# Optimization experiments

Measured on AMD Instinct MI355X. Metric: run time of the kernel, lower is better.

## Reference

```python
import jax, jax.numpy as jnp
import numpy as np

D_STATE = 8
DT_RANK = 8  # ceil(128/16)


def _grouped_1x1(x, w):
    # x: (B,H,W,Cin), w: (g, Cout//g, Cin//g)
    B, H, W, _ = x.shape
    g, o, i = w.shape
    xg = x.reshape(B, H, W, g, i)
    return jnp.einsum('bhwgi,goi->bhwgo', xg, w).reshape(B, H, W, g * o)


def setup_inputs() -> dict:
    key = jax.random.key(0)
    ks = jax.random.split(key, 16)
    B, H, W, C = 8, 64, 64, 128
    g = 4
    D = 128  # expand_dim = d_inner
    N = D_STATE
    R = DT_RANK
    inp = {}
    inp['x'] = jax.random.normal(ks[0], (B, H, W, C), dtype=jnp.float32)
    inp['w1'] = jax.random.normal(ks[1], (g, D // g, C // g), dtype=jnp.float32) * 0.1
    inp['dw'] = jax.random.normal(ks[2], (3, 3, 1, D), dtype=jnp.float32) * 0.1  # HWIO depthwise
    inp['in_proj_w'] = jax.random.normal(ks[3], (2 * D, D), dtype=jnp.float32) * 0.05
    inp['conv1d_w'] = jax.random.normal(ks[4], (D, 3), dtype=jnp.float32) * 0.1
    inp['conv1d_b'] = jax.random.normal(ks[5], (D,), dtype=jnp.float32) * 0.05
    inp['x_proj_w'] = jax.random.normal(ks[6], (R + 2 * N, D), dtype=jnp.float32) * 0.05
    inp['dt_proj_w'] = jax.random.normal(ks[7], (D, R), dtype=jnp.float32) * 0.05
    inp['dt_proj_b'] = jax.random.normal(ks[8], (D,), dtype=jnp.float32) * 0.05
    inp['A_log'] = jnp.log(jnp.tile(jnp.arange(1, N + 1, dtype=jnp.float32)[None, :], (D, 1)))
    inp['D_param'] = jnp.ones((D,), dtype=jnp.float32)
    inp['out_proj_w'] = jax.random.normal(ks[9], (D, D), dtype=jnp.float32) * 0.05
    inp['gamma'] = jnp.ones((D,), dtype=jnp.float32)
    inp['beta'] = jnp.zeros((D,), dtype=jnp.float32)
    inp['w2'] = jax.random.normal(ks[10], (g, D // g, C // g), dtype=jnp.float32) * 0.1
    inp['wout'] = jax.random.normal(ks[11], (g, C // g, D // g), dtype=jnp.float32) * 0.1
    return inp


def _mamba(x_seq, in_proj_w, conv1d_w, conv1d_b, x_proj_w, dt_proj_w, dt_proj_b, A_log, D_param, out_proj_w):
    # x_seq: (B, L, D)
    B, L, D = x_seq.shape
    N, R = D_STATE, DT_RANK
    xz = jnp.einsum('bld,ed->ble', x_seq, in_proj_w)  # (B,L,2D)
    u, z = xz[..., :D], xz[..., D:]
    # causal depthwise conv1d, kernel=3, left pad 2 (torch: padding=2, slice [:L])
    up = jnp.pad(u, ((0, 0), (2, 0), (0, 0)))
    u = (up[:, 0:L] * conv1d_w[:, 0] + up[:, 1:L + 1] * conv1d_w[:, 1]
         + up[:, 2:L + 2] * conv1d_w[:, 2] + conv1d_b)
    u = jax.nn.silu(u)
    x_dbl = jnp.einsum('bld,ed->ble', u, x_proj_w)  # (B,L,R+2N)
    dt = x_dbl[..., :R]
    Bm = x_dbl[..., R:R + N]
    Cm = x_dbl[..., R + N:]
    delta = jax.nn.softplus(jnp.einsum('blr,dr->bld', dt, dt_proj_w) + dt_proj_b)  # (B,L,D)
    A = -jnp.exp(A_log)  # (D,N)

    def step(h, inp):
        d_t, u_t, b_t, c_t = inp  # (B,D),(B,D),(B,N),(B,N)
        dA = jnp.exp(d_t[..., None] * A)            # (B,D,N)
        h = dA * h + (d_t * u_t)[..., None] * b_t[:, None, :]
        y_t = jnp.einsum('bdn,bn->bd', h, c_t)
        return h, y_t

    h0 = jnp.zeros((B, D, N), dtype=x_seq.dtype)
    xs = (jnp.swapaxes(delta, 0, 1), jnp.swapaxes(u, 0, 1),
          jnp.swapaxes(Bm, 0, 1), jnp.swapaxes(Cm, 0, 1))
    _, ys = jax.lax.scan(step, h0, xs)              # ys: (L,B,D)
    y = jnp.swapaxes(ys, 0, 1) + u * D_param
    y = y * jax.nn.silu(z)
    return jnp.einsum('bld,ed->ble', y, out_proj_w)


def reference(x, w1, dw, in_proj_w, conv1d_w, conv1d_b, x_proj_w, dt_proj_w, dt_proj_b,
              A_log, D_param, out_proj_w, gamma, beta, w2, wout):
    B, H, W, C = x.shape
    D = dw.shape[-1]
    x1 = _grouped_1x1(x, w1)  # (B,H,W,D)
    x1 = jax.lax.conv_general_dilated(
        x1, dw, window_strides=(1, 1), padding='SAME',
        feature_group_count=D, dimension_numbers=('NHWC', 'HWIO', 'NHWC'))
    x1 = jax.nn.silu(x1)
    x1_seq = x1.reshape(B, H * W, D)
    x1_seq = _mamba(x1_seq, in_proj_w, conv1d_w, conv1d_b, x_proj_w,
                    dt_proj_w, dt_proj_b, A_log, D_param, out_proj_w)
    x1 = x1_seq.reshape(B, H, W, D)
    mu = jnp.mean(x1, axis=-1, keepdims=True)
    var = jnp.mean(jnp.square(x1 - mu), axis=-1, keepdims=True)
    x1 = (x1 - mu) * jax.lax.rsqrt(var + 1e-5) * gamma + beta
    x2 = jax.nn.silu(_grouped_1x1(x, w2))
    x_fuse = x1 * x2
    return _grouped_1x1(x_fuse, wout)  # (B,H,W,C)
```

## Files before the change

kernel.cpp:

```cpp
#include <hip/hip_runtime.h>
#include <math.h>

#define B_    8
#define C_    128
#define D_    128
#define L_    4096
#define NPOS_ 32768
#define NC_   256
#define S_    16
#define MFL_  1048576

typedef __attribute__((ext_vector_type(8))) short short8;
typedef __attribute__((ext_vector_type(4))) float f32x4;

__device__ __forceinline__ float siluf(float x) { return x / (1.f + __expf(-x)); }
__device__ __forceinline__ float softplusf(float x) {
    if (x > 20.f) return x;
    return __logf(1.f + __expf(x));
}
__device__ __forceinline__ unsigned short f2bf(float f) {
    unsigned int u = __float_as_uint(f);
    u = (u + 0x7FFFu + ((u >> 16) & 1u)) >> 16;
    return (unsigned short)u;
}
__device__ __forceinline__ float bf2f(unsigned short h) {
    return __uint_as_float(((unsigned int)h) << 16);
}
__device__ __forceinline__ void scan_as(float dl, const float* Ar, bool fast, float* a) {
    if (fast) {
        float e1 = __expf(-dl);
        a[0] = e1;
        a[1] = e1 * e1;
        a[2] = a[1] * e1;
        a[3] = a[1] * a[1];
        a[4] = a[3] * e1;
        a[5] = a[3] * a[1];
        a[6] = a[5] * e1;
        a[7] = a[3] * a[3];
    } else {
        #pragma unroll
        for (int n = 0; n < 8; ++n) a[n] = __expf(dl * Ar[n]);
    }
}

__global__ __launch_bounds__(256) void k1_g1x1(const float* __restrict__ x,
                                               const float* __restrict__ w1,
                                               const float* __restrict__ w2,
                                               const float* __restrict__ inW,
                                               const float* __restrict__ OW,
                                               const float* __restrict__ xpw,
                                               unsigned short* __restrict__ inWb,
                                               unsigned short* __restrict__ OWb,
                                               unsigned short* __restrict__ xpwb,
                                               unsigned short* __restrict__ t1b,
                                               unsigned short* __restrict__ x2sb) {
    __shared__ float xs[16 * 128];
    int t = threadIdx.x;
    {
        int i = blockIdx.x * 51 + t;
        if (t < 51 && i < 52224) {
            if (i < 32768)      inWb[i] = f2bf(inW[i]);
            else if (i < 49152) OWb[i - 32768] = f2bf(OW[i - 32768]);
            else                xpwb[i - 49152] = f2bf(xpw[i - 49152]);
        }
    }
    int op = t & 63, ph = t >> 6;
    int g = op >> 4, o2 = (op & 15) * 2;
    const float* w1p = &w1[g * 1024 + o2 * 32];
    const float* w2p = &w2[g * 1024 + o2 * 32];
    float w1r[64], w2r[64];
    #pragma unroll
    for (int i = 0; i < 64; ++i) { w1r[i] = w1p[i]; w2r[i] = w2p[i]; }
    int pos0 = blockIdx.x * 32;
    for (int it = 0; it < 2; ++it) {
        int p0 = pos0 + it * 16;
        #pragma unroll
        for (int q = 0; q < 2; ++q) {
            int fi = t * 2 + q;
            *(float4*)&xs[fi * 4] = *(const float4*)&x[p0 * 128 + fi * 4];
        }
        __syncthreads();
        #pragma unroll
        for (int q = 0; q < 4; ++q) {
            int pl = ph * 4 + q;
            float a1 = 0.f, b1 = 0.f, a2 = 0.f, b2 = 0.f;
            const float* xr = &xs[pl * 128 + g * 32];
            #pragma unroll
            for (int i4 = 0; i4 < 8; ++i4) {
                float4 xv = *(const float4*)&xr[i4 * 4];
                a1 += xv.x * w1r[i4*4]    + xv.y * w1r[i4*4+1]    + xv.z * w1r[i4*4+2]    + xv.w * w1r[i4*4+3];
                b1 += xv.x * w1r[32+i4*4] + xv.y * w1r[32+i4*4+1] + xv.z * w1r[32+i4*4+2] + xv.w * w1r[32+i4*4+3];
                a2 += xv.x * w2r[i4*4]    + xv.y * w2r[i4*4+1]    + xv.z * w2r[i4*4+2]    + xv.w * w2r[i4*4+3];
                b2 += xv.x * w2r[32+i4*4] + xv.y * w2r[32+i4*4+1] + xv.z * w2r[32+i4*4+2] + xv.w * w2r[32+i4*4+3];
            }
            int pos = p0 + pl;
            int db = pos * 128 + g * 32 + o2;
            unsigned int u1 = (unsigned int)f2bf(a1) | ((unsigned int)f2bf(b1) << 16);
            unsigned int u2 = (unsigned int)f2bf(siluf(a2)) | ((unsigned int)f2bf(siluf(b2)) << 16);
            *(unsigned int*)&t1b[db]  = u1;
            *(unsigned int*)&x2sb[db] = u2;
        }
        __syncthreads();
    }
}

__global__ __launch_bounds__(128) void k2_dwconv(const unsigned short* __restrict__ t1b,
                                                 const float* __restrict__ dw,
                                                 unsigned short* __restrict__ x1cb) {
    int d = threadIdx.x;
    float dwr[9];
    #pragma unroll
    for (int k = 0; k < 9; ++k) dwr[k] = dw[k * 128 + d];
    int bid = blockIdx.x;
    int wt = bid & 15, ht = (bid >> 4) & 7, b = bid >> 7;
    int h0 = ht * 8, w0 = wt * 4;
    float rows[10][6];
    #pragma unroll
    for (int r = 0; r < 10; ++r) {
        int hh = h0 - 1 + r;
        bool hv = (hh >= 0) && (hh < 64);
        #pragma unroll
        for (int c = 0; c < 6; ++c) {
            int w = w0 - 1 + c;
            bool wvv = (w >= 0) && (w < 64);
            rows[r][c] = (hv && wvv) ? bf2f(t1b[((b * 64 + hh) * 64 + w) * 128 + d]) : 0.f;
        }
    }
    #pragma unroll
    for (int hi = 0; hi < 8; ++hi) {
        #pragma unroll
        for (int wi = 0; wi < 4; ++wi) {
            float acc = rows[hi][wi]     * dwr[0] + rows[hi][wi+1]   * dwr[1] + rows[hi][wi+2]   * dwr[2]
                      + rows[hi+1][wi]   * dwr[3] + rows[hi+1][wi+1] * dwr[4] + rows[hi+1][wi+2] * dwr[5]
                      + rows[hi+2][wi]   * dwr[6] + rows[hi+2][wi+1] * dwr[7] + rows[hi+2][wi+2] * dwr[8];
            x1cb[((b * 64 + h0 + hi) * 64 + w0 + wi) * 128 + d] = f2bf(siluf(acc));
        }
    }
}

__global__ __launch_bounds__(256) void k3_mfma(const unsigned short* __restrict__ Abf,
                                               const unsigned short* __restrict__ Bbf,
                                               unsigned short* __restrict__ urawb,
                                               unsigned short* __restrict__ zb) {
    __shared__ unsigned short Al[64 * 72];
    __shared__ unsigned short Bl[128 * 72];
    int t = threadIdx.x;
    int pos0 = (blockIdx.x >> 1) * 64;
    int half = blockIdx.x & 1;
    const unsigned short* Bh = Bbf + (size_t)half * 128 * 128;
    unsigned short* dst = half ? zb : urawb;
    int lane = t & 63, wv = t >> 6;
    int lanem = lane & 15, laneq = lane >> 4;
    f32x4 acc[8];
    #pragma unroll
    for (int i = 0; i < 8; ++i) acc[i] = (f32x4){0.f, 0.f, 0.f, 0.f};
    for (int kc = 0; kc < 2; ++kc) {
        #pragma unroll
        for (int q = 0; q < 2; ++q) {
            int c = t + q * 256;
            int row = c >> 3, col = c & 7;
            *(int4*)&Al[row * 72 + col * 8] = *(const int4*)&Abf[(pos0 + row) * 128 + kc * 64 + col * 8];
        }
        #pragma unroll
        for (int q = 0; q < 4; ++q) {
            int c = t + q * 256;
            int row = c >> 3, col = c & 7;
            *(int4*)&Bl[row * 72 + col * 8] = *(const int4*)&Bh[row * 128 + kc * 64 + col * 8];
        }
        __syncthreads();
        #pragma unroll
        for (int ks = 0; ks < 2; ++ks) {
            short8 af = *(const short8*)&Al[(wv * 16 + lanem) * 72 + ks * 32 + laneq * 8];
            #pragma unroll
            for (int ni = 0; ni < 8; ++ni) {
                short8 bfr = *(const short8*)&Bl[(ni * 16 + lanem) * 72 + ks * 32 + laneq * 8];
                acc[ni] = __builtin_amdgcn_mfma_f32_16x16x32_bf16(af, bfr, acc[ni], 0, 0, 0);
            }
        }
        __syncthreads();
    }
    #pragma unroll
    for (int ni = 0; ni < 8; ++ni)
        #pragma unroll
        for (int r = 0; r < 4; ++r) {
            int m = pos0 + wv * 16 + laneq * 4 + r;
            int n = ni * 16 + lanem;
            dst[m * 128 + n] = f2bf(acc[ni][r]);
        }
}

__global__ __launch_bounds__(256) void k45_convproj(const unsigned short* __restrict__ urawb,
                                                    const float* __restrict__ cw,
                                                    const float* __restrict__ cb,
                                                    const unsigned short* __restrict__ xpwb,
                                                    const float* __restrict__ dtw,
                                                    const float* __restrict__ dtb,
                                                    const float* __restrict__ A_log,
                                                    unsigned short* __restrict__ usb,
                                                    unsigned short* __restrict__ deltab,
                                                    float* __restrict__ Bm,
                                                    float* __restrict__ Cm,
                                                    float* __restrict__ cA,
                                                    float* __restrict__ cB) {
    __shared__ unsigned short uA[32 * 136];
    __shared__ unsigned short xB[32 * 136];
    __shared__ float xdb[32 * 36];
    int t = threadIdx.x;
    int d = t & 127, ph = t >> 7;
    for (int i = t; i < 32 * 128; i += 256) {
        int n = i >> 7, k = i & 127;
        xB[n * 136 + k] = (n < 24) ? xpwb[n * 128 + k] : (unsigned short)0;
    }
    float cw0 = cw[d * 3 + 0], cw1 = cw[d * 3 + 1], cw2 = cw[d * 3 + 2], cbr = cb[d];
    float dtwr[8];
    #pragma unroll
    for (int r = 0; r < 8; ++r) dtwr[r] = dtw[d * 8 + r];
    float dtbr = dtb[d];
    float Ar[8]; bool fast = true;
    #pragma unroll
    for (int n = 0; n < 8; ++n) {
        Ar[n] = -__expf(A_log[d * 8 + n]);
        fast = fast && (fabsf(Ar[n] + (float)(n + 1)) < 2e-3f);
    }

    int gpos0 = blockIdx.x * 32;
    int ll0 = (gpos0 & 4095) + ph * 16;
    int base = (gpos0 + ph * 16) * 128 + d;
    float ur0 = (ll0 >= 2) ? bf2f(urawb[base - 256]) : 0.f;
    float ur1 = (ll0 >= 1) ? bf2f(urawb[base - 128]) : 0.f;
    #pragma unroll
    for (int q = 0; q < 16; ++q) {
        float urq = bf2f(urawb[base + q * 128]);
        float v = siluf(ur0 * cw0 + ur1 * cw1 + urq * cw2 + cbr);
        unsigned short vb = f2bf(v);
        usb[base + q * 128] = vb;
        uA[(ph * 16 + q) * 136 + d] = vb;
        ur0 = ur1; ur1 = urq;
    }
    __syncthreads();
    int lane = t & 63, wv = t >> 6;
    int lanem = lane & 15, laneq = lane >> 4;
    int m0 = (wv & 1) * 16, n0 = (wv >> 1) * 16;
    f32x4 accx = (f32x4){0.f, 0.f, 0.f, 0.f};
    #pragma unroll
    for (int ks = 0; ks < 4; ++ks) {
        short8 af  = *(const short8*)&uA[(m0 + lanem) * 136 + ks * 32 + laneq * 8];
        short8 bfr = *(const short8*)&xB[(n0 + lanem) * 136 + ks * 32 + laneq * 8];
        accx = __builtin_amdgcn_mfma_f32_16x16x32_bf16(af, bfr, accx, 0, 0, 0);
    }
    #pragma unroll
    for (int r = 0; r < 4; ++r)
        xdb[(m0 + laneq * 4 + r) * 36 + n0 + lanem] = accx[r];
    __syncthreads();
    float h[8], ap[8];
    #pragma unroll
    for (int n = 0; n < 8; ++n) { h[n] = 0.f; ap[n] = 1.f; }
    #pragma unroll
    for (int q = 0; q < 16; ++q) {
        int pl = ph * 16 + q;
        const float* xrow = &xdb[pl * 36];
        float4 d0 = *(const float4*)&xrow[0];
        float4 d1 = *(const float4*)&xrow[4];
        float dt = dtbr + d0.x * dtwr[0] + d0.y * dtwr[1] + d0.z * dtwr[2] + d0.w * dtwr[3]
                        + d1.x * dtwr[4] + d1.y * dtwr[5] + d1.z * dtwr[6] + d1.w * dtwr[7];
        unsigned short dlb = f2bf(softplusf(dt));
        deltab[base + q * 128] = dlb;
        float dl = bf2f(dlb);
        float du = dl * bf2f(uA[pl * 136 + d]);
        float bmv[8];
        *(float4*)&bmv[0] = *(const float4*)&xrow[8];
        *(float4*)&bmv[4] = *(const float4*)&xrow[12];
        float a[8];
        scan_as(dl, Ar, fast, a);
        #pragma unroll
        for (int n = 0; n < 8; ++n) {
            ap[n] *= a[n];
            h[n] = a[n] * h[n] + du * bmv[n];
        }
    }
    int bH = gpos0 >> 12;
    int c  = ((gpos0 & 4095) >> 4) + ph;
    int obase = ((bH * NC_ + c) * 128 + d) * 8;
    *(float4*)&cA[obase]     = make_float4(ap[0], ap[1], ap[2], ap[3]);
    *(float4*)&cA[obase + 4] = make_float4(ap[4], ap[5], ap[6], ap[7]);
    *(float4*)&cB[obase]     = make_float4(h[0], h[1], h[2], h[3]);
    *(float4*)&cB[obase + 4] = make_float4(h[4], h[5], h[6], h[7]);
    if (t < 128) {
        int p = t >> 2, q = t & 3;
        float4 v = *(const float4*)&xdb[p * 36 + 8 + q * 4];
        int gp = gpos0 + p;
        if (q < 2) *(float4*)&Bm[gp * 8 + q * 4] = v;
        else       *(float4*)&Cm[gp * 8 + (q - 2) * 4] = v;
    }
}

__global__ __launch_bounds__(256) void k6a_scan(float* __restrict__ cA,
                                                float* __restrict__ cB,
                                                float* __restrict__ AgA,
                                                float* __restrict__ AgB) {
    int id = blockIdx.x * 256 + threadIdx.x;
    int dn = id & 1023;
    int grp = (id >> 10) & 15;
    int b = id >> 14;
    float Apre = 1.f, h = 0.f;
    int base = (b * NC_ + grp * 16) * 1024 + dn;
    #pragma unroll 4
    for (int j = 0; j < 16; ++j) {
        int idx = base + j * 1024;
        float a  = cA[idx];
        float bv = cB[idx];
        cA[idx] = Apre;
        cB[idx] = h;
        Apre *= a;
        h = a * h + bv;
    }
    int aidx = (b * 16 + grp) * 1024 + dn;
    AgA[aidx] = Apre;
    AgB[aidx] = h;
}

__global__ __launch_bounds__(256) void k6b_scan(const float* __restrict__ AgA,
                                                const float* __restrict__ AgB,
                                                float* __restrict__ gcar) {
    int id = blockIdx.x * 256 + threadIdx.x;
    int dn = id & 1023;
    int b = id >> 10;
    float h = 0.f;
    #pragma unroll
    for (int grp = 0; grp < 16; ++grp) {
        int idx = (b * 16 + grp) * 1024 + dn;
        float Ag = AgA[idx];
        float Bg = AgB[idx];
        gcar[idx] = h;
        h = Ag * h + Bg;
    }
}

__global__ __launch_bounds__(512) void k7f_fused(const unsigned short* __restrict__ deltab,
                                                 const unsigned short* __restrict__ usb,
                                                 const float* __restrict__ Bm,
                                                 const float* __restrict__ Cm,
                                                 const unsigned short* __restrict__ zb,
                                                 const float* __restrict__ A_log,
                                                 const float* __restrict__ Dp,
                                                 const float* __restrict__ Apre,
                                                 const float* __restrict__ Bpre,
                                                 const float* __restrict__ gcar,
                                                 const unsigned short* __restrict__ OWb,
                                                 const float* __restrict__ gamma,
                                                 const float* __restrict__ beta,
                                                 const unsigned short* __restrict__ x2sb,
                                                 const float* __restrict__ wout,
                                                 float* __restrict__ out) {
    __shared__ __align__(16) char smem[37888];
    unsigned short* yA = (unsigned short*)smem;
    unsigned short* Bl = (unsigned short*)(smem + 18432);
    float* xz = (float*)smem;
    __shared__ float woutL[4 * 1160];
    __shared__ float gbL[256];
    int t = threadIdx.x;
    for (int idx = t; idx < 4096; idx += 512) {
        int g = idx >> 10, r = idx & 1023, o = r >> 5, i = r & 31;
        woutL[g * 1160 + o * 36 + i] = wout[idx];
    }
    if (t < 128) gbL[t] = gamma[t];
    else if (t < 256) gbL[t] = beta[t - 128];

    int d = t & 127, ph = t >> 7;
    int b = blockIdx.x >> 6, cblk = blockIdx.x & 63;
    float Ar[8]; bool fast = true;
    #pragma unroll
    for (int n = 0; n < 8; ++n) {
        Ar[n] = -__expf(A_log[d * 8 + n]);
        fast = fast && (fabsf(Ar[n] + (float)(n + 1)) < 2e-3f);
    }
    float Dpr = Dp[d];
    int ybase = (d >> 6) * (64 * 72) + (d & 63);
    {
        int cl = ph;
        int c = cblk * 4 + cl;
        int cbase = ((b * NC_ + c) * 128 + d) * 8;
        float4 ap0 = *(const float4*)&Apre[cbase];
        float4 ap1 = *(const float4*)&Apre[cbase + 4];
        float4 bp0 = *(const float4*)&Bpre[cbase];
        float4 bp1 = *(const float4*)&Bpre[cbase + 4];
        int gbase = (b * 16 + (c >> 4)) * 1024 + d * 8;
        float4 g0 = *(const float4*)&gcar[gbase];
        float4 g1 = *(const float4*)&gcar[gbase + 4];
        float h[8] = { fmaf(g0.x, ap0.x, bp0.x), fmaf(g0.y, ap0.y, bp0.y),
                       fmaf(g0.z, ap0.z, bp0.z), fmaf(g0.w, ap0.w, bp0.w),
                       fmaf(g1.x, ap1.x, bp1.x), fmaf(g1.y, ap1.y, bp1.y),
                       fmaf(g1.z, ap1.z, bp1.z), fmaf(g1.w, ap1.w, bp1.w) };
        int base  = (b * L_ + c * S_) * 128 + d;
        int bbase = (b * L_ + c * S_) * 8;
        #pragma unroll
        for (int s = 0; s < S_; ++s) {
            float dl = bf2f(deltab[base + s * 128]);
            float uv = bf2f(usb[base + s * 128]);
            float zv = bf2f(zb[base + s * 128]);
            float du = dl * uv;
            float4 bm0 = *(const float4*)&Bm[bbase + s * 8];
            float4 bm1 = *(const float4*)&Bm[bbase + s * 8 + 4];
            float4 cm0 = *(const float4*)&Cm[bbase + s * 8];
            float4 cm1 = *(const float4*)&Cm[bbase + s * 8 + 4];
            float a[8];
            scan_as(dl, Ar, fast, a);
            h[0] = a[0] * h[0] + du * bm0.x;
            h[1] = a[1] * h[1] + du * bm0.y;
            h[2] = a[2] * h[2] + du * bm0.z;
            h[3] = a[3] * h[3] + du * bm0.w;
            h[4] = a[4] * h[4] + du * bm1.x;
            h[5] = a[5] * h[5] + du * bm1.y;
            h[6] = a[6] * h[6] + du * bm1.z;
            h[7] = a[7] * h[7] + du * bm1.w;
            float yv = h[0] * cm0.x + h[1] * cm0.y + h[2] * cm0.z + h[3] * cm0.w
                     + h[4] * cm1.x + h[5] * cm1.y + h[6] * cm1.z + h[7] * cm1.w;
            yv = (yv + uv * Dpr) * siluf(zv);
            yA[ybase + (cl * 16 + s) * 72] = f2bf(yv);
        }
    }
    __syncthreads();

    int lane = t & 63, wv = t >> 6;
    int lanem = lane & 15, laneq = lane >> 4;
    int mi = wv & 3, nb = (wv >> 2) * 4;
    f32x4 acc[4];
    #pragma unroll
    for (int i = 0; i < 4; ++i) acc[i] = (f32x4){0.f, 0.f, 0.f, 0.f};
    for (int kc = 0; kc < 2; ++kc) {
        #pragma unroll
        for (int q = 0; q < 2; ++q) {
            int cidx = t + q * 512;
            int row = cidx >> 3, col = cidx & 7;
            *(int4*)&Bl[row * 72 + col * 8] = *(const int4*)&OWb[row * 128 + kc * 64 + col * 8];
        }
        __syncthreads();
        #pragma unroll
        for (int ks = 0; ks < 2; ++ks) {
            short8 af = *(const short8*)&yA[kc * (64 * 72) + (mi * 16 + lanem) * 72 + ks * 32 + laneq * 8];
            #pragma unroll
            for (int ni = 0; ni < 4; ++ni) {
                short8 bfr = *(const short8*)&Bl[((nb + ni) * 16 + lanem) * 72 + ks * 32 + laneq * 8];
                acc[ni] = __builtin_amdgcn_mfma_f32_16x16x32_bf16(af, bfr, acc[ni], 0, 0, 0);
            }
        }
        __syncthreads();
    }
    #pragma unroll
    for (int ni = 0; ni < 4; ++ni) {
        int ch = (nb + ni) * 16 + lanem;
        int col = ch + ((ch >> 5) << 2);
        #pragma unroll
        for (int r = 0; r < 4; ++r)
            xz[(mi * 16 + laneq * 4 + r) * 148 + col] = bf2f(f2bf(acc[ni][r]));
    }
    __syncthreads();

    if (t < 256) {
        int g = t & 3, pos = t >> 2;
        int gpos = b * L_ + cblk * 64 + pos;
        const float* xrow0 = &xz[pos * 148 + g * 36];
        float v[32];
        #pragma unroll
        for (int i4 = 0; i4 < 8; ++i4) {
            float4 xv = *(const float4*)&xrow0[i4 * 4];
            v[i4*4+0] = xv.x; v[i4*4+1] = xv.y;
            v[i4*4+2] = xv.z; v[i4*4+3] = xv.w;
        }
        float s = 0.f, s2 = 0.f;
        #pragma unroll
        for (int i = 0; i < 32; ++i) { s += v[i]; s2 += v[i] * v[i]; }
        s  += __shfl_xor(s, 1, 64);  s  += __shfl_xor(s, 2, 64);
        s2 += __shfl_xor(s2, 1, 64); s2 += __shfl_xor(s2, 2, 64);
        float m = s * (1.f / 128.f);
        float var = s2 * (1.f / 128.f) - m * m;
        float rstd = rsqrtf(var + 1e-5f);
        #pragma unroll
        for (int i4 = 0; i4 < 8; ++i4) {
            ushort4 xv = *(const ushort4*)&x2sb[gpos * 128 + g * 32 + i4 * 4];
            unsigned short xa[4] = {xv.x, xv.y, xv.z, xv.w};
            #pragma unroll
            for (int k = 0; k < 4; ++k) {
                int e = g * 32 + i4 * 4 + k;
                float vv = (v[i4 * 4 + k] - m) * rstd * gbL[e] + gbL[128 + e];
                v[i4 * 4 + k] = vv * bf2f(xa[k]);
            }
        }
        const float* wg = &woutL[g * 1160];
        int obase = gpos * 128 + g * 32;
        #pragma unroll
        for (int ob = 0; ob < 8; ++ob) {
            float o4[4];
            #pragma unroll
            for (int oo = 0; oo < 4; ++oo) {
                int o = ob * 4 + oo;
                float acc2 = 0.f;
                #pragma unroll
                for (int i4 = 0; i4 < 8; ++i4) {
                    float4 wv4 = *(const float4*)&wg[o * 36 + i4 * 4];
                    acc2 += v[i4*4] * wv4.x + v[i4*4+1] * wv4.y
                          + v[i4*4+2] * wv4.z + v[i4*4+3] * wv4.w;
                }
                o4[oo] = acc2;
            }
            *(float4*)&out[obase + ob * 4] = make_float4(o4[0], o4[1], o4[2], o4[3]);
        }
    }
}

extern "C" void kernel_launch(void* const* d_in, const int* in_sizes, int n_in,
                              void* d_out, int out_size, void* d_ws, size_t ws_size,
                              hipStream_t stream) {
    (void)in_sizes; (void)n_in; (void)out_size; (void)ws_size;
    const float* x         = (const float*)d_in[0];
    const float* w1        = (const float*)d_in[1];
    const float* dw        = (const float*)d_in[2];
    const float* in_proj_w = (const float*)d_in[3];
    const float* conv1d_w  = (const float*)d_in[4];
    const float* conv1d_b  = (const float*)d_in[5];
    const float* x_proj_w  = (const float*)d_in[6];
    const float* dt_proj_w = (const float*)d_in[7];
    const float* dt_proj_b = (const float*)d_in[8];
    const float* A_log     = (const float*)d_in[9];
    const float* D_param   = (const float*)d_in[10];
    const float* out_proj_w= (const float*)d_in[11];
    const float* gamma     = (const float*)d_in[12];
    const float* beta      = (const float*)d_in[13];
    const float* w2        = (const float*)d_in[14];
    const float* wout      = (const float*)d_in[15];
    float* out = (float*)d_out;

    float* ws = (float*)d_ws;
    unsigned short* x2sb   = (unsigned short*)(ws);
    unsigned short* t1b    = (unsigned short*)(ws + 2  * (size_t)MFL_);
    unsigned short* x1cb   = (unsigned short*)(ws + 4  * (size_t)MFL_);
    unsigned short* urawb  = (unsigned short*)(ws + 6  * (size_t)MFL_);
    unsigned short* zb     = (unsigned short*)(ws + 8  * (size_t)MFL_);
    unsigned short* usb    = (unsigned short*)(ws + 14 * (size_t)MFL_);
    unsigned short* deltab = (unsigned short*)(ws + 16 * (size_t)MFL_);
    float* Bm    = ws + 18 * (size_t)MFL_;
    float* Cm    = Bm + (size_t)NPOS_ * 8;
    float* cA    = Cm + (size_t)NPOS_ * 8;
    float* cB    = cA + 2 * (size_t)MFL_;
    float* scanw = cB + 2 * (size_t)MFL_;
    float* AgA   = scanw;
    float* AgB   = scanw + 131072;
    float* gcar  = scanw + 262144;
    unsigned short* inWb = (unsigned short*)(scanw + 2 * (size_t)MFL_);
    unsigned short* OWb  = inWb + 32768;
    unsigned short* xpwb = OWb + 16384;

    k1_g1x1<<<1024, 256, 0, stream>>>(x, w1, w2, in_proj_w, out_proj_w, x_proj_w,
                                      inWb, OWb, xpwb, t1b, x2sb);
    k2_dwconv<<<1024, 128, 0, stream>>>(t1b, dw, x1cb);
    k3_mfma<<<1024, 256, 0, stream>>>(x1cb, inWb, urawb, zb);
    k45_convproj<<<1024, 256, 0, stream>>>(urawb, conv1d_w, conv1d_b, xpwb,
                                           dt_proj_w, dt_proj_b, A_log,
                                           usb, deltab, Bm, Cm, cA, cB);
    k6a_scan<<<512, 256, 0, stream>>>(cA, cB, AgA, AgB);
    k6b_scan<<<32, 256, 0, stream>>>(AgA, AgB, gcar);
    k7f_fused<<<512, 512, 0, stream>>>(deltab, usb, Bm, Cm, zb, A_log, D_param,
                                       cA, cB, gcar, OWb, gamma, beta, x2sb, wout, out);
}
```

Measured before the change: 213.4 us.

## Fuse depthwise conv into in_proj MFMA kernel via shared-memory A tile

Merges the depthwise 3x3 conv + SiLU kernel with the in_proj MFMA GEMM. Each 512-thread block computes one image row (64 positions) of conv output straight into LDS, then eight waves compute both the u and z halves from that tile. This removes the x1cb global write/read round trip and one launch. In exchange it changes the block shape, uses a sliding-window conv along w that re-reads neighbouring rows from global, and raises LDS use per block.

```diff
diff --git a/kernel.cpp b/kernel.cpp
--- a/kernel.cpp
+++ b/kernel.cpp
@@ -104,76 +104,80 @@
     }
 }
 
-__global__ __launch_bounds__(128) void k2_dwconv(const unsigned short* __restrict__ t1b,
-                                                 const float* __restrict__ dw,
-                                                 unsigned short* __restrict__ x1cb) {
-    int d = threadIdx.x;
-    float dwr[9];
-    #pragma unroll
-    for (int k = 0; k < 9; ++k) dwr[k] = dw[k * 128 + d];
+__global__ __launch_bounds__(512) void k23_dwmfma(const unsigned short* __restrict__ t1b,
+                                                  const float* __restrict__ dw,
+                                                  const unsigned short* __restrict__ Bbf,
+                                                  unsigned short* __restrict__ urawb,
+                                                  unsigned short* __restrict__ zb) {
+    __shared__ __align__(16) unsigned short Ax[64 * 136];
+    __shared__ __align__(16) unsigned short Bl[2 * 128 * 72];
+    int t = threadIdx.x;
     int bid = blockIdx.x;
-    int wt = bid & 15, ht = (bid >> 4) & 7, b = bid >> 7;
-    int h0 = ht * 8, w0 = wt * 4;
-    float rows[10][6];
-    #pragma unroll
-    for (int r = 0; r < 10; ++r) {
-        int hh = h0 - 1 + r;
-        bool hv = (hh >= 0) && (hh < 64);
-        #pragma unroll
-        for (int c = 0; c < 6; ++c) {
-            int w = w0 - 1 + c;
-            bool wvv = (w >= 0) && (w < 64);
-            rows[r][c] = (hv && wvv) ? bf2f(t1b[((b * 64 + hh) * 64 + w) * 128 + d]) : 0.f;
-        }
-    }
-    #pragma unroll
-    for (int hi = 0; hi < 8; ++hi) {
-        #pragma unroll
-        for (int wi = 0; wi < 4; ++wi) {
-            float acc = rows[hi][wi]     * dwr[0] + rows[hi][wi+1]   * dwr[1] + rows[hi][wi+2]   * dwr[2]
-                      + rows[hi+1][wi]   * dwr[3] + rows[hi+1][wi+1] * dwr[4] + rows[hi+1][wi+2] * dwr[5]
-                      + rows[hi+2][wi]   * dwr[6] + rows[hi+2][wi+1] * dwr[7] + rows[hi+2][wi+2] * dwr[8];
-            x1cb[((b * 64 + h0 + hi) * 64 + w0 + wi) * 128 + d] = f2bf(siluf(acc));
-        }
-    }
-}
-
-__global__ __launch_bounds__(256) void k3_mfma(const unsigned short* __restrict__ Abf,
-                                               const unsigned short* __restrict__ Bbf,
-                                               unsigned short* __restrict__ urawb,
-                                               unsigned short* __restrict__ zb) {
-    __shared__ unsigned short Al[64 * 72];
-    __shared__ unsigned short Bl[128 * 72];
-    int t = threadIdx.x;
-    int pos0 = (blockIdx.x >> 1) * 64;
-    int half = blockIdx.x & 1;
-    const unsigned short* Bh = Bbf + (size_t)half * 128 * 128;
-    unsigned short* dst = half ? zb : urawb;
+    int h = bid & 63, b = bid >> 6;
+
+    {
+        int d = t & 127, wq = t >> 7;
+        float dwr[9];
+        #pragma unroll
+        for (int k = 0; k < 9; ++k) dwr[k] = dw[k * 128 + d];
+        int w0 = wq * 16;
+        bool h0v = (h - 1) >= 0, h2v = (h + 1) < 64;
+        int rowbase = ((b * 64 + h) * 64) * 128 + d;
+        float a0, a1, a2, b0, b1, b2, c0, c1, c2;
+        {
+            int ww = w0 - 1;
+            bool wvv = ww >= 0;
+            a0 = (wvv && h0v) ? bf2f(t1b[rowbase + (ww - 64) * 128]) : 0.f;
+            a1 =  wvv         ? bf2f(t1b[rowbase +  ww       * 128]) : 0.f;
+            a2 = (wvv && h2v) ? bf2f(t1b[rowbase + (ww + 64) * 128]) : 0.f;
+        }
+        {
+            int ww = w0;
+            b0 = h0v ? bf2f(t1b[rowbase + (ww - 64) * 128]) : 0.f;
+            b1 =       bf2f(t1b[rowbase +  ww       * 128]);
+            b2 = h2v ? bf2f(t1b[rowbase + (ww + 64) * 128]) : 0.f;
+        }
+        #pragma unroll
+        for (int wi = 0; wi < 16; ++wi) {
+            int w = w0 + wi;
+            int ww = w + 1;
+            bool wvv = ww < 64;
+            c0 = (wvv && h0v) ? bf2f(t1b[rowbase + (ww - 64) * 128]) : 0.f;
+            c1 =  wvv         ? bf2f(t1b[rowbase +  ww       * 128]) : 0.f;
+            c2 = (wvv && h2v) ? bf2f(t1b[rowbase + (ww + 64) * 128]) : 0.f;
+            float acc = a0 * dwr[0] + b0 * dwr[1] + c0 * dwr[2]
+                      + a1 * dwr[3] + b1 * dwr[4] + c1 * dwr[5]
+                      + a2 * dwr[6] + b2 * dwr[7] + c2 * dwr[8];
+            Ax[w * 136 + d] = f2bf(siluf(acc));
+            a0 = b0; a1 = b1; a2 = b2;
+            b0 = c0; b1 = c1; b2 = c2;
+        }
+    }
+    __syncthreads();
+
     int lane = t & 63, wv = t >> 6;
     int lanem = lane & 15, laneq = lane >> 4;
+    int wvm = wv & 3, half = wv >> 2;
+    unsigned short* dst = half ? zb : urawb;
     f32x4 acc[8];
     #pragma unroll
     for (int i = 0; i < 8; ++i) acc[i] = (f32x4){0.f, 0.f, 0.f, 0.f};
     for (int kc = 0; kc < 2; ++kc) {
         #pragma unroll
-        for (int q = 0; q < 2; ++q) {
-            int c = t + q * 256;
-            int row = c >> 3, col = c & 7;
-            *(int4*)&Al[row * 72 + col * 8] = *(const int4*)&Abf[(pos0 + row) * 128 + kc * 64 + col * 8];
-        }
-        #pragma unroll
         for (int q = 0; q < 4; ++q) {
-            int c = t + q * 256;
-            int row = c >> 3, col = c & 7;
-            *(int4*)&Bl[row * 72 + col * 8] = *(const int4*)&Bh[row * 128 + kc * 64 + col * 8];
+            int cidx = t + q * 512;
+            int hb = cidx >> 10, r2 = cidx & 1023;
+            int row = r2 >> 3, col = r2 & 7;
+            *(int4*)&Bl[(hb * 128 + row) * 72 + col * 8] =
+                *(const int4*)&Bbf[hb * 16384 + row * 128 + kc * 64 + col * 8];
         }
         __syncthreads();
         #pragma unroll
         for (int ks = 0; ks < 2; ++ks) {
-            short8 af = *(const short8*)&Al[(wv * 16 + lanem) * 72 + ks * 32 + laneq * 8];
+            short8 af = *(const short8*)&Ax[(wvm * 16 + lanem) * 136 + kc * 64 + ks * 32 + laneq * 8];
             #pragma unroll
             for (int ni = 0; ni < 8; ++ni) {
-                short8 bfr = *(const short8*)&Bl[(ni * 16 + lanem) * 72 + ks * 32 + laneq * 8];
+                short8 bfr = *(const short8*)&Bl[(half * 128 + ni * 16 + lanem) * 72 + ks * 32 + laneq * 8];
                 acc[ni] = __builtin_amdgcn_mfma_f32_16x16x32_bf16(af, bfr, acc[ni], 0, 0, 0);
             }
         }
@@ -183,7 +187,7 @@
     for (int ni = 0; ni < 8; ++ni)
         #pragma unroll
         for (int r = 0; r < 4; ++r) {
-            int m = pos0 + wv * 16 + laneq * 4 + r;
+            int m = bid * 64 + wvm * 16 + laneq * 4 + r;
             int n = ni * 16 + lanem;
             dst[m * 128 + n] = f2bf(acc[ni][r]);
         }
@@ -533,7 +537,6 @@
     float* ws = (float*)d_ws;
     unsigned short* x2sb   = (unsigned short*)(ws);
     unsigned short* t1b    = (unsigned short*)(ws + 2  * (size_t)MFL_);
-    unsigned short* x1cb   = (unsigned short*)(ws + 4  * (size_t)MFL_);
     unsigned short* urawb  = (unsigned short*)(ws + 6  * (size_t)MFL_);
     unsigned short* zb     = (unsigned short*)(ws + 8  * (size_t)MFL_);
     unsigned short* usb    = (unsigned short*)(ws + 14 * (size_t)MFL_);
@@ -552,8 +555,7 @@
 
     k1_g1x1<<<1024, 256, 0, stream>>>(x, w1, w2, in_proj_w, out_proj_w, x_proj_w,
                                       inWb, OWb, xpwb, t1b, x2sb);
-    k2_dwconv<<<1024, 128, 0, stream>>>(t1b, dw, x1cb);
-    k3_mfma<<<1024, 256, 0, stream>>>(x1cb, inWb, urawb, zb);
+    k23_dwmfma<<<512, 512, 0, stream>>>(t1b, dw, inWb, urawb, zb);
     k45_convproj<<<1024, 256, 0, stream>>>(urawb, conv1d_w, conv1d_b, xpwb,
                                            dt_proj_w, dt_proj_b, A_log,
                                            usb, deltab, Bm, Cm, cA, cB);
```

Measured after the change: 214.9 us. Within noise of the previous version (+0.7%).
